# Kernel tuning notes

Hardware: AMD Instinct MI355X
Metric: run time of the kernel (lower is better)

The kernel has to match this reference:

```python
import jax, jax.numpy as jnp
import numpy as np

B, T, LATENT, FFN, TEMB = 4, 4096, 256, 1024, 2048
D = 8 * LATENT  # 2048
LN_EPS = 1e-5


def setup_inputs() -> dict:
    key = jax.random.key(0)
    ks = jax.random.split(key, 12)
    s1 = 1.0 / np.sqrt(LATENT)
    s2 = 1.0 / np.sqrt(FFN)
    sd = 1.0 / np.sqrt(D)
    st = 1.0 / np.sqrt(TEMB)
    return {
        "x": jax.random.normal(ks[0], (B, T, D), dtype=jnp.float32),
        "emb": jax.random.normal(ks[1], (B, TEMB), dtype=jnp.float32),
        # 8 parallel branch weights, batched along leading expert axis
        "W1": jax.random.uniform(ks[2], (8, LATENT, FFN), jnp.float32, -s1, s1),
        "b1": jax.random.uniform(ks[3], (8, FFN), jnp.float32, -s1, s1),
        "W2": jax.random.uniform(ks[4], (8, FFN, LATENT), jnp.float32, -s2, s2),
        "b2": jax.random.uniform(ks[5], (8, LATENT), jnp.float32, -s2, s2),
        # StylizationBlock params (latent_dim*8 = D)
        "emb_W": jax.random.uniform(ks[6], (TEMB, 2 * D), jnp.float32, -st, st),
        "emb_b": jax.random.uniform(ks[7], (2 * D,), jnp.float32, -st, st),
        "ln_g": jnp.ones((D,), jnp.float32),
        "ln_b": jnp.zeros((D,), jnp.float32),
        "out_W": jax.random.uniform(ks[8], (D, D), jnp.float32, -sd, sd),
        "out_b": jax.random.uniform(ks[9], (D,), jnp.float32, -sd, sd),
    }


def _layernorm(h, g, b):
    mu = jnp.mean(h, axis=-1, keepdims=True)
    var = jnp.mean(jnp.square(h - mu), axis=-1, keepdims=True)
    return (h - mu) * jax.lax.rsqrt(var + LN_EPS) * g + b


def reference(x, emb, W1, b1, W2, b2, emb_W, emb_b, ln_g, ln_b, out_W, out_b):
    Bx, Tx, Dx = x.shape
    xr = x.reshape(Bx, Tx, 8, LATENT)  # (B,T,8,latent)
    # 8 parallel Linear->GELU->Linear chains as batched GEMMs
    h = jnp.einsum("btel,elf->btef", xr, W1) + b1  # (B,T,8,ffn)
    h = jax.nn.gelu(h, approximate=False)  # dropout=0 (eval)
    y = jnp.einsum("btef,efl->btel", h, W2) + b2  # (B,T,8,latent)
    y = y.reshape(Bx, Tx, Dx)  # concat along channels
    # StylizationBlock: scale/shift from time emb, LN, SiLU, Linear
    eo = jax.nn.silu(emb) @ emb_W + emb_b  # (B, 2D)
    scale, shift = jnp.split(eo[:, None, :], 2, axis=-1)  # (B,1,D) each
    hn = _layernorm(y, ln_g, ln_b) * (1.0 + scale) + shift
    proj = jax.nn.silu(hn) @ out_W + out_b  # (B,T,D)
    return x + proj
```

## Files before the change

### kernel.cpp

```cpp
#include <hip/hip_runtime.h>

typedef __attribute__((ext_vector_type(8))) __bf16 bf16x8;
typedef __attribute__((ext_vector_type(4))) __bf16 bf16x4;
typedef __attribute__((ext_vector_type(4))) float f32x4;

#define TOKENS 16384
#define DDIM   2048
#define LAT    256
#define FFND   1024

__device__ __forceinline__ void gload_lds16(const __bf16* g, __bf16* l) {
  __builtin_amdgcn_global_load_lds(
      (const __attribute__((address_space(1))) void*)g,
      (__attribute__((address_space(3))) void*)l, 16, 0, 0);
}

__global__ void transpose_f32_bf16(const float* __restrict__ src, __bf16* __restrict__ dst,
                                   int R, int C) {
  __shared__ float tile[32][33];
  const int b = blockIdx.z;
  src += (size_t)b * R * C;
  dst += (size_t)b * R * C;
  const int c0 = blockIdx.x * 32, r0 = blockIdx.y * 32;
  const int tx = threadIdx.x & 31, ty = threadIdx.x >> 5;
  for (int i = ty; i < 32; i += 8)
    tile[i][tx] = src[(size_t)(r0 + i) * C + c0 + tx];
  __syncthreads();
  for (int i = ty; i < 32; i += 8)
    dst[(size_t)(c0 + i) * R + r0 + tx] = (__bf16)tile[tx][i];
}

__global__ void k0_partial(const float* __restrict__ emb, const float* __restrict__ embW,
                           float* __restrict__ pp) {
  __shared__ float se[4 * 256];
  const int tid = threadIdx.x;
  const int kc = blockIdx.y;
  const int kb = kc * 256;
  for (int i = tid; i < 1024; i += 256) {
    const int bb = i >> 8, kk = i & 255;
    float v = emb[bb * 2048 + kb + kk];
    se[i] = v / (1.f + __expf(-v));
  }
  __syncthreads();
  const int j = blockIdx.x * 256 + tid;
  float a0 = 0.f, a1 = 0.f, a2 = 0.f, a3 = 0.f;
  for (int k = 0; k < 256; ++k) {
    float wv = embW[(size_t)(kb + k) * 4096 + j];
    a0 += se[k] * wv;
    a1 += se[256 + k] * wv;
    a2 += se[512 + k] * wv;
    a3 += se[768 + k] * wv;
  }
  pp[(size_t)(kc * 4 + 0) * 4096 + j] = a0;
  pp[(size_t)(kc * 4 + 1) * 4096 + j] = a1;
  pp[(size_t)(kc * 4 + 2) * 4096 + j] = a2;
  pp[(size_t)(kc * 4 + 3) * 4096 + j] = a3;
}

__global__ void k0_reduce(const float* __restrict__ pp, const float* __restrict__ embb,
                          float* __restrict__ ss) {
  const int j = blockIdx.x * 256 + threadIdx.x;
  const float bb = embb[j];
#pragma unroll
  for (int b = 0; b < 4; ++b) {
    float s = bb;
#pragma unroll
    for (int kc = 0; kc < 8; ++kc) s += pp[(size_t)(kc * 4 + b) * 4096 + j];
    ss[b * 4096 + j] = s;
  }
}

__device__ __forceinline__ void gemm_acc(const __bf16* __restrict__ wsrc, int wstride,
                                         const __bf16* lds, int swz, int ln, int q,
                                         f32x4 (&acc)[2][4]) {
#pragma unroll
  for (int k0 = 0; k0 < 256; k0 += 32) {
    bf16x8 af[4], bfr[2];
#pragma unroll
    for (int j = 0; j < 2; ++j)
      bfr[j] = *(const bf16x8*)(wsrc + (size_t)(j * 16 + ln) * wstride + k0 + q * 8);
#pragma unroll
    for (int i = 0; i < 4; ++i)
      af[i] = *(const bf16x8*)(lds + (i * 16 + ln) * 256 + ((k0 + q * 8) ^ swz));
#pragma unroll
    for (int j = 0; j < 2; ++j)
#pragma unroll
      for (int i = 0; i < 4; ++i)
        acc[j][i] = __builtin_amdgcn_mfma_f32_16x16x32_bf16(bfr[j], af[i], acc[j][i], 0, 0, 0);
  }
}

__launch_bounds__(512, 4)
__global__ void k1_expert_ffn(const float* __restrict__ x, const __bf16* __restrict__ W1T,
                              const float* __restrict__ b1, const __bf16* __restrict__ W2T,
                              const float* __restrict__ b2, __bf16* __restrict__ y) {
  __shared__ __bf16 xs[64 * 256];
  __shared__ __bf16 hs[64 * 256];

  const int tid = threadIdx.x;
  const int w = tid >> 6;
  const int lane = tid & 63;
  const int q = lane >> 4;
  const int ln = lane & 15;
  const int m0 = blockIdx.x * 64;
  const int e = blockIdx.y;
  const int swz = (ln & 7) << 3;

  {
    const int r0 = tid >> 6;
    const int c = (tid & 63) * 4;
#pragma unroll
    for (int p = 0; p < 8; ++p) {
      const int r = r0 + p * 8;
      f32x4 v = *(const f32x4*)(x + (size_t)(m0 + r) * DDIM + e * LAT + c);
      bf16x4 o;
      o[0] = (__bf16)v[0]; o[1] = (__bf16)v[1]; o[2] = (__bf16)v[2]; o[3] = (__bf16)v[3];
      *(bf16x4*)(xs + r * 256 + (c ^ ((r & 7) << 3))) = o;
    }
  }

  f32x4 acc_y[2][4];
#pragma unroll
  for (int j = 0; j < 2; ++j) {
    f32x4 bv = *(const f32x4*)(b2 + e * LAT + w * 32 + j * 16 + q * 4);
#pragma unroll
    for (int i = 0; i < 4; ++i) acc_y[j][i] = bv;
  }

  f32x4 acc_h[2][4];

  __syncthreads();

#pragma unroll
  for (int j = 0; j < 2; ++j) {
    f32x4 bv = *(const f32x4*)(b1 + e * FFND + w * 32 + j * 16 + q * 4);
#pragma unroll
    for (int i = 0; i < 4; ++i) acc_h[j][i] = bv;
  }
  gemm_acc(W1T + ((size_t)e * FFND + w * 32) * LAT, LAT, xs, swz, ln, q, acc_h);

  for (int fc = 0; fc < 4; ++fc) {
#pragma unroll
    for (int j = 0; j < 2; ++j)
#pragma unroll
      for (int i = 0; i < 4; ++i) {
        const int tok = i * 16 + ln;
        const int fcol = w * 32 + j * 16 + q * 4;
        bf16x4 o;
#pragma unroll
        for (int r = 0; r < 4; ++r) {
          float vv = acc_h[j][i][r];
          float u2 = -1.5957691216057308f * vv * (1.0f + 0.044715f * vv * vv);
          u2 = fminf(u2, 80.f);
          float ge = vv * __builtin_amdgcn_rcpf(1.0f + __expf(u2));
          o[r] = (__bf16)ge;
        }
        *(bf16x4*)(hs + tok * 256 + (fcol ^ ((tok & 7) << 3))) = o;
      }

    __syncthreads();

    if (fc < 3) {
#pragma unroll
      for (int j = 0; j < 2; ++j) {
        f32x4 bv = *(const f32x4*)(b1 + e * FFND + (fc + 1) * 256 + w * 32 + j * 16 + q * 4);
#pragma unroll
        for (int i = 0; i < 4; ++i) acc_h[j][i] = bv;
      }
      gemm_acc(W1T + ((size_t)e * FFND + (fc + 1) * 256 + w * 32) * LAT, LAT,
               xs, swz, ln, q, acc_h);
    }

    gemm_acc(W2T + ((size_t)(e * LAT + w * 32)) * FFND + fc * 256, FFND,
             hs, swz, ln, q, acc_y);

    __syncthreads();
  }

#pragma unroll
  for (int j = 0; j < 2; ++j)
#pragma unroll
    for (int i = 0; i < 4; ++i) {
      const int tok = i * 16 + ln;
      const int l = w * 32 + j * 16 + q * 4;
      bf16x4 o;
#pragma unroll
      for (int r = 0; r < 4; ++r) o[r] = (__bf16)acc_y[j][i][r];
      *(bf16x4*)(y + (size_t)(m0 + tok) * DDIM + e * LAT + l) = o;
    }
}

__global__ void k2_ln_mod_silu(const float* __restrict__ ss, const float* __restrict__ g,
                               const float* __restrict__ bb, __bf16* __restrict__ y) {
  __shared__ float red[8];
  const int t = blockIdx.x;
  const int b = t >> 12;
  const int tid = threadIdx.x;
  __bf16* row = y + (size_t)t * DDIM;
  bf16x8 v8 = *(bf16x8*)(row + tid * 8);
  float v[8], s = 0.f, sq = 0.f;
#pragma unroll
  for (int i = 0; i < 8; ++i) {
    v[i] = (float)v8[i];
    s += v[i];
    sq += v[i] * v[i];
  }
#pragma unroll
  for (int off = 32; off > 0; off >>= 1) {
    s += __shfl_down(s, off);
    sq += __shfl_down(sq, off);
  }
  if ((tid & 63) == 0) {
    red[tid >> 6] = s;
    red[4 + (tid >> 6)] = sq;
  }
  __syncthreads();
  const float S = red[0] + red[1] + red[2] + red[3];
  const float SQ = red[4] + red[5] + red[6] + red[7];
  const float mean = S * (1.f / DDIM);
  const float var = SQ * (1.f / DDIM) - mean * mean;
  const float rstd = rsqrtf(var + 1e-5f);
  const float* sc = ss + (size_t)b * 2 * DDIM;
#pragma unroll
  for (int i = 0; i < 8; ++i) {
    const int d = tid * 8 + i;
    float hn = (v[i] - mean) * rstd * g[d] + bb[d];
    hn = hn * (1.f + sc[d]) + sc[DDIM + d];
    float si = hn / (1.f + __expf(-hn));
    v8[i] = (__bf16)si;
  }
  *(bf16x8*)(row + tid * 8) = v8;
}

__launch_bounds__(256, 2)
__global__ void k3_proj(const __bf16* __restrict__ a, const __bf16* __restrict__ oWT,
                        const float* __restrict__ ob, const float* __restrict__ x,
                        float* __restrict__ out, int m_base) {
  __shared__ __bf16 As[128 * 64];
  __shared__ __bf16 Bs[128 * 64];
  const int tid = threadIdx.x;
  const int w = tid >> 6, lane = tid & 63, q = lane >> 4, ln = lane & 15;
  const int wm = w >> 1, wn = w & 1;
  const int m0 = m_base + blockIdx.x * 128, n0 = blockIdx.y * 128;
  const int swz = (ln & 7) << 3;
  const int rr = lane >> 3;
  const int co = ((lane & 7) ^ rr) * 8;
  f32x4 acc[4][4] = {};

  for (int k0 = 0; k0 < 2048; k0 += 64) {
    __syncthreads();
#pragma unroll
    for (int p = 0; p < 4; ++p) {
      const int rbase = w * 32 + p * 8;
      gload_lds16(a   + (size_t)(m0 + rbase + rr) * DDIM + k0 + co, As + rbase * 64);
      gload_lds16(oWT + (size_t)(n0 + rbase + rr) * DDIM + k0 + co, Bs + rbase * 64);
    }
    __syncthreads();
#pragma unroll
    for (int ks = 0; ks < 64; ks += 32) {
      bf16x8 af[4], bfr[4];
#pragma unroll
      for (int i = 0; i < 4; ++i)
        af[i] = *(const bf16x8*)(As + (wm * 64 + i * 16 + ln) * 64 + ((ks + q * 8) ^ swz));
#pragma unroll
      for (int j = 0; j < 4; ++j)
        bfr[j] = *(const bf16x8*)(Bs + (wn * 64 + j * 16 + ln) * 64 + ((ks + q * 8) ^ swz));
#pragma unroll
      for (int j = 0; j < 4; ++j)
#pragma unroll
        for (int i = 0; i < 4; ++i)
          acc[j][i] = __builtin_amdgcn_mfma_f32_16x16x32_bf16(bfr[j], af[i], acc[j][i], 0, 0, 0);
    }
  }

#pragma unroll
  for (int j = 0; j < 4; ++j) {
    const int n = n0 + wn * 64 + j * 16 + q * 4;
    const f32x4 bn4 = *(const f32x4*)(ob + n);
#pragma unroll
    for (int i = 0; i < 4; ++i) {
      const int m = m0 + wm * 64 + i * 16 + ln;
      const f32x4 xr = *(const f32x4*)(x + (size_t)m * DDIM + n);
      f32x4 v;
#pragma unroll
      for (int r = 0; r < 4; ++r) v[r] = acc[j][i][r] + bn4[r] + xr[r];
      *(f32x4*)(out + (size_t)m * DDIM + n) = v;
    }
  }
}

extern "C" void kernel_launch(void* const* d_in, const int* in_sizes, int n_in,
                              void* d_out, int out_size, void* d_ws, size_t ws_size,
                              hipStream_t stream) {
  const float* x    = (const float*)d_in[0];
  const float* emb  = (const float*)d_in[1];
  const float* W1   = (const float*)d_in[2];
  const float* b1   = (const float*)d_in[3];
  const float* W2   = (const float*)d_in[4];
  const float* b2   = (const float*)d_in[5];
  const float* embW = (const float*)d_in[6];
  const float* embb = (const float*)d_in[7];
  const float* lng  = (const float*)d_in[8];
  const float* lnb  = (const float*)d_in[9];
  const float* outW = (const float*)d_in[10];
  const float* outb = (const float*)d_in[11];
  float* out = (float*)d_out;

  char* ob = (char*)d_out;
  __bf16* W1T  = (__bf16*)ob;
  __bf16* W2T  = (__bf16*)(ob + (4 << 20));
  float*  pp   = (float*)(ob + (8 << 20));
  float*  ss   = (float*)(ob + (8 << 20) + (512 << 10));
  __bf16* oWT1 = (__bf16*)ob;
  __bf16* y    = (__bf16*)d_ws;
  __bf16* oWT2 = (__bf16*)((char*)d_ws + (8 << 20));

  transpose_f32_bf16<<<dim3(32, 8, 8), 256, 0, stream>>>(W1, W1T, 256, 1024);
  transpose_f32_bf16<<<dim3(8, 32, 8), 256, 0, stream>>>(W2, W2T, 1024, 256);
  k0_partial<<<dim3(16, 8), 256, 0, stream>>>(emb, embW, pp);
  k0_reduce<<<16, 256, 0, stream>>>(pp, embb, ss);
  k1_expert_ffn<<<dim3(TOKENS / 64, 8), 512, 0, stream>>>(x, W1T, b1, W2T, b2, y);
  k2_ln_mod_silu<<<TOKENS, 256, 0, stream>>>(ss, lng, lnb, y);
  transpose_f32_bf16<<<dim3(64, 64, 1), 256, 0, stream>>>(outW, oWT1, 2048, 2048);
  k3_proj<<<dim3(112, 16), 256, 0, stream>>>(y, oWT1, outb, x, out, 2048);
  transpose_f32_bf16<<<dim3(64, 64, 1), 256, 0, stream>>>(outW, oWT2, 2048, 2048);
  k3_proj<<<dim3(16, 16), 256, 0, stream>>>(y, oWT2, outb, x, out, 0);
}
```

Before: 792.8 us.

## Preload weight fragments into registers before barriers in expert FFN kernel

The per-K-step global weight loads inside the GEMM helper are replaced by a bulk preload of all 16 bf16x8 weight fragments into registers. The load is issued ahead of the barrier so its latency can overlap the sync and GELU writes. The W2 GEMM is moved ahead of the next W1 GEMM. Launch bounds drop from 4 to 2 blocks per SM to make room for the extra registers, which costs occupancy.

```diff
diff --git a/kernel.cpp b/kernel.cpp
--- a/kernel.cpp
+++ b/kernel.cpp
@@ -70,27 +70,32 @@
   }
 }
 
-__device__ __forceinline__ void gemm_acc(const __bf16* __restrict__ wsrc, int wstride,
-                                         const __bf16* lds, int swz, int ln, int q,
-                                         f32x4 (&acc)[2][4]) {
-#pragma unroll
-  for (int k0 = 0; k0 < 256; k0 += 32) {
-    bf16x8 af[4], bfr[2];
+__device__ __forceinline__ void wload(const __bf16* __restrict__ wsrc, int wstride,
+                                      int ln, int q, bf16x8 (&bw)[16]) {
+#pragma unroll
+  for (int k0 = 0; k0 < 8; ++k0)
 #pragma unroll
     for (int j = 0; j < 2; ++j)
-      bfr[j] = *(const bf16x8*)(wsrc + (size_t)(j * 16 + ln) * wstride + k0 + q * 8);
+      bw[k0 * 2 + j] = *(const bf16x8*)(wsrc + (size_t)(j * 16 + ln) * wstride + k0 * 32 + q * 8);
+}
+
+__device__ __forceinline__ void gemm_pre(const bf16x8 (&bw)[16], const __bf16* lds,
+                                         int swz, int ln, int q, f32x4 (&acc)[2][4]) {
+#pragma unroll
+  for (int k0 = 0; k0 < 8; ++k0) {
+    bf16x8 af[4];
 #pragma unroll
     for (int i = 0; i < 4; ++i)
-      af[i] = *(const bf16x8*)(lds + (i * 16 + ln) * 256 + ((k0 + q * 8) ^ swz));
+      af[i] = *(const bf16x8*)(lds + (i * 16 + ln) * 256 + ((k0 * 32 + q * 8) ^ swz));
 #pragma unroll
     for (int j = 0; j < 2; ++j)
 #pragma unroll
       for (int i = 0; i < 4; ++i)
-        acc[j][i] = __builtin_amdgcn_mfma_f32_16x16x32_bf16(bfr[j], af[i], acc[j][i], 0, 0, 0);
-  }
-}
-
-__launch_bounds__(512, 4)
+        acc[j][i] = __builtin_amdgcn_mfma_f32_16x16x32_bf16(bw[k0 * 2 + j], af[i], acc[j][i], 0, 0, 0);
+  }
+}
+
+__launch_bounds__(512, 2)
 __global__ void k1_expert_ffn(const float* __restrict__ x, const __bf16* __restrict__ W1T,
                               const float* __restrict__ b1, const __bf16* __restrict__ W2T,
                               const float* __restrict__ b2, __bf16* __restrict__ y) {
@@ -128,6 +133,9 @@
   }
 
   f32x4 acc_h[2][4];
+  bf16x8 bw[16];
+
+  wload(W1T + ((size_t)e * FFND + w * 32) * LAT, LAT, ln, q, bw);
 
   __syncthreads();
 
@@ -137,7 +145,7 @@
 #pragma unroll
     for (int i = 0; i < 4; ++i) acc_h[j][i] = bv;
   }
-  gemm_acc(W1T + ((size_t)e * FFND + w * 32) * LAT, LAT, xs, swz, ln, q, acc_h);
+  gemm_pre(bw, xs, swz, ln, q, acc_h);
 
   for (int fc = 0; fc < 4; ++fc) {
 #pragma unroll
@@ -158,21 +166,22 @@
         *(bf16x4*)(hs + tok * 256 + (fcol ^ ((tok & 7) << 3))) = o;
       }
 
+    wload(W2T + ((size_t)(e * LAT + w * 32)) * FFND + fc * 256, FFND, ln, q, bw);
+
     __syncthreads();
 
+    gemm_pre(bw, hs, swz, ln, q, acc_y);
+
     if (fc < 3) {
+      wload(W1T + ((size_t)e * FFND + (fc + 1) * 256 + w * 32) * LAT, LAT, ln, q, bw);
 #pragma unroll
       for (int j = 0; j < 2; ++j) {
         f32x4 bv = *(const f32x4*)(b1 + e * FFND + (fc + 1) * 256 + w * 32 + j * 16 + q * 4);
 #pragma unroll
         for (int i = 0; i < 4; ++i) acc_h[j][i] = bv;
       }
-      gemm_acc(W1T + ((size_t)e * FFND + (fc + 1) * 256 + w * 32) * LAT, LAT,
-               xs, swz, ln, q, acc_h);
-    }
-
-    gemm_acc(W2T + ((size_t)(e * LAT + w * 32)) * FFND + fc * 256, FFND,
-             hs, swz, ln, q, acc_y);
+      gemm_pre(bw, xs, swz, ln, q, acc_h);
+    }
 
     __syncthreads();
   }
```

Result: no change. 801.9 us (+1.2%).
